# Performance work log

Measured on AMD Instinct MI355X. Metric: run time of the kernel, lower is better.

Reference implementation:

```python
import jax, jax.numpy as jnp
import numpy as np

L, N, C = 128, 32, 128
DIM_MLP, OUT = 128, 128


def setup_inputs() -> dict:
    key = jax.random.key(0)
    ks = jax.random.split(key, 6)
    s_in2 = 1.0 / np.sqrt(2 * C)
    s_mid = 1.0 / np.sqrt(DIM_MLP)
    s_in = 1.0 / np.sqrt(C)
    return {
        "x": jax.random.normal(ks[0], (L, N, C), jnp.float32),
        "attn_w1": jax.random.normal(ks[1], (2 * C, DIM_MLP), jnp.float32) * s_in2,
        "attn_b1": jnp.zeros((DIM_MLP,), jnp.float32),
        "attn_w2": jax.random.normal(ks[2], (DIM_MLP, OUT), jnp.float32) * s_mid,
        "attn_b2": jnp.zeros((OUT,), jnp.float32),
        "value_w1": jax.random.normal(ks[3], (C, DIM_MLP), jnp.float32) * s_in,
        "value_b1": jnp.zeros((DIM_MLP,), jnp.float32),
        "value_w2": jax.random.normal(ks[4], (DIM_MLP, OUT), jnp.float32) * s_mid,
        "value_b2": jnp.zeros((OUT,), jnp.float32),
    }


def reference(x, attn_w1, attn_b1, attn_w2, attn_b2,
              value_w1, value_b1, value_w2, value_b2):
    l, n, c = x.shape
    # Outer concat: pair[i, j, b] = concat(x[i, b], x[j, b])  -> (l, l, N, 2C)
    xi = jnp.broadcast_to(x[:, None, :, :], (l, l, n, c))
    xj = jnp.broadcast_to(x[None, :, :, :], (l, l, n, c))
    pair = jnp.concatenate([xi, xj], axis=-1)
    # Pairwise attention MLP (ReLU hidden, linear output)
    h = jax.nn.relu(pair @ attn_w1 + attn_b1)          # (l, l, N, dim_mlp)
    attn = h @ attn_w2 + attn_b2                       # (l, l, N, out)
    # Value MLP
    hv = jax.nn.relu(x @ value_w1 + value_b1)          # (l, N, dim_mlp)
    value = hv @ value_w2 + value_b2                   # (l, N, out)
    # Elementwise weighted reduce over key axis j (NOT a matmul over channels)
    out = jnp.einsum('ijbc,jbc->ibc', attn, value)     # (l, N, out)
    return out
```

## Files before the change

kernel.cpp:

```cpp
#include <hip/hip_runtime.h>
#include <hip/hip_bf16.h>

#define L_DIM 128
#define N_DIM 32
#define C_DIM 128
#define K_DIM 128
#define OUT_DIM 128

#define QV_STRIDE 132

typedef __attribute__((ext_vector_type(8))) short short8;
typedef __attribute__((ext_vector_type(4))) float float4v;

static __device__ __forceinline__ short bf16_bits(float f) {
    __bf16 h = (__bf16)f;
    return __builtin_bit_cast(short, h);
}

__global__ __launch_bounds__(256) void k_pre(
    const float* __restrict__ x,
    const float* __restrict__ attn_w1, const float* __restrict__ attn_b1,
    const float* __restrict__ attn_w2,
    const float* __restrict__ value_w1, const float* __restrict__ value_b1,
    const float* __restrict__ value_w2, const float* __restrict__ value_b2,
    float* __restrict__ P, float* __restrict__ Q, float* __restrict__ V,
    short* __restrict__ W2s)
{
    int bid = blockIdx.x;
    if (bid >= 256) {
        int e = (bid - 256) * 256 + threadIdx.x;
        int idx  = e & 7;
        int colr = (e >> 3) & 15;
        int quad = (e >> 7) & 3;
        int mi   = (e >> 9) & 3;
        int ct   = e >> 11;
        int k = quad * 8 + 32 * mi + idx;
        int c = ct * 16 + colr;
        W2s[e] = bf16_bits(attn_w2[k * OUT_DIM + c]);
        return;
    }

    __shared__ float xs[16][C_DIM];
    __shared__ float hvs[16][K_DIM];
    int tid = threadIdx.x;
    int r0  = bid * 16;

    {
        int f = tid * 8;
        int row = f >> 7, c = f & 127;
        *(float4v*)(&xs[row][c])     = *(const float4v*)(x + (r0 + row) * C_DIM + c);
        *(float4v*)(&xs[row][c + 4]) = *(const float4v*)(x + (r0 + row) * C_DIM + c + 4);
    }
    __syncthreads();

    int ks   = tid & 127;
    int half = tid >> 7;

    float pacc[8] = {0,0,0,0,0,0,0,0};
    float qacc[8] = {0,0,0,0,0,0,0,0};
    float hacc[8] = {0,0,0,0,0,0,0,0};
    #pragma unroll 4
    for (int c = 0; c < C_DIM; ++c) {
        float wa = attn_w1[c * K_DIM + ks];
        float wb = attn_w1[(C_DIM + c) * K_DIM + ks];
        float wv = value_w1[c * K_DIM + ks];
        #pragma unroll
        for (int r = 0; r < 8; ++r) {
            float xr = xs[half * 8 + r][c];
            pacc[r] = fmaf(xr, wa, pacc[r]);
            qacc[r] = fmaf(xr, wb, qacc[r]);
            hacc[r] = fmaf(xr, wv, hacc[r]);
        }
    }
    float b1 = attn_b1[ks], vb1 = value_b1[ks];
    #pragma unroll
    for (int r = 0; r < 8; ++r) {
        int rr = r0 + half * 8 + r;
        int i = rr >> 5, bb = rr & 31;
        P[(bb * L_DIM + i) * K_DIM + ks] = pacc[r];
        Q[(bb * L_DIM + i) * K_DIM + ks] = qacc[r] + b1;
        hvs[half * 8 + r][ks] = fmaxf(hacc[r] + vb1, 0.f);
    }
    __syncthreads();

    float vacc[8] = {0,0,0,0,0,0,0,0};
    #pragma unroll 4
    for (int k = 0; k < K_DIM; ++k) {
        float w = value_w2[k * OUT_DIM + ks];
        #pragma unroll
        for (int r = 0; r < 8; ++r)
            vacc[r] = fmaf(hvs[half * 8 + r][k], w, vacc[r]);
    }
    float vb2 = value_b2[ks];
    #pragma unroll
    for (int r = 0; r < 8; ++r) {
        int rr = r0 + half * 8 + r;
        int i = rr >> 5, bb = rr & 31;
        V[(bb * L_DIM + i) * OUT_DIM + ks] = vacc[r] + vb2;
    }
}

__global__ __launch_bounds__(256)
__attribute__((amdgpu_waves_per_eu(2, 2)))
void k_main(
    const float* __restrict__ P, const float* __restrict__ Q,
    const float* __restrict__ V,
    const short* __restrict__ W2s, const float* __restrict__ attn_b2,
    float* __restrict__ out)
{
    __shared__ float Q_lds[2][16 * QV_STRIDE];
    __shared__ float V_lds[2][16 * QV_STRIDE];
    __shared__ float P_lds[8 * K_DIM];

    int b     = blockIdx.x >> 4;
    int itile = blockIdx.x & 15;
    int tid   = threadIdx.x;
    int wave  = tid >> 6;
    int lane  = tid & 63;
    int quad  = lane >> 4;
    int col   = lane & 15;

    short8 bfrag[8][4];
    const short8* w2p = (const short8*)W2s;
    #pragma unroll
    for (int ct = 0; ct < 8; ++ct)
        #pragma unroll
        for (int mi = 0; mi < 4; ++mi)
            bfrag[ct][mi] = w2p[((ct * 4 + mi) * 4 + quad) * 16 + col];

    {
        int f = tid * 4;
        int ii = f >> 7, k = f & 127;
        *(float4v*)&P_lds[f] =
            *(const float4v*)(P + (b * L_DIM + itile * 8 + ii) * K_DIM + k);
    }

    int srow = tid >> 4;
    int sc8  = (tid & 15) * 8;
    const float* Qbase = Q + (size_t)(b * L_DIM) * K_DIM;
    const float* Vbase = V + (size_t)(b * L_DIM) * OUT_DIM;

    {
        const float* qp = Qbase + srow * K_DIM + sc8;
        const float* vp = Vbase + srow * OUT_DIM + sc8;
        float4v qa = *(const float4v*)qp, qb = *(const float4v*)(qp + 4);
        float4v va = *(const float4v*)vp, vb = *(const float4v*)(vp + 4);
        *(float4v*)&Q_lds[0][srow * QV_STRIDE + sc8]     = qa;
        *(float4v*)&Q_lds[0][srow * QV_STRIDE + sc8 + 4] = qb;
        *(float4v*)&V_lds[0][srow * QV_STRIDE + sc8]     = va;
        *(float4v*)&V_lds[0][srow * QV_STRIDE + sc8 + 4] = vb;
    }
    __syncthreads();

    float acc[2][8] = {};
    float sv[8]     = {};

    for (int r = 0; r < 8; ++r) {
        int cur = r & 1;

        short8 af[2][4];
        const float* Qc = &Q_lds[cur][col * QV_STRIDE + quad * 8];
        #pragma unroll
        for (int ksl = 0; ksl < 4; ++ksl) {
            float4v q0 = *(const float4v*)(Qc + ksl * 32);
            float4v q1 = *(const float4v*)(Qc + ksl * 32 + 4);
            #pragma unroll
            for (int ii = 0; ii < 2; ++ii) {
                const float* Pc =
                    &P_lds[(wave * 2 + ii) * K_DIM + ksl * 32 + quad * 8];
                float4v pa = *(const float4v*)Pc;
                float4v pb = *(const float4v*)(Pc + 4);
                float4v sa = pa + q0;
                float4v sb = pb + q1;
                short8 a;
                #pragma unroll
                for (int t = 0; t < 4; ++t) {
                    a[t]     = bf16_bits(fmaxf(sa[t], 0.f));
                    a[t + 4] = bf16_bits(fmaxf(sb[t], 0.f));
                }
                af[ii][ksl] = a;
            }
        }

        float4v nqa, nqb, nva, nvb;
        if (r < 7) {
            const float* qp = Qbase + ((r + 1) * 16 + srow) * K_DIM + sc8;
            const float* vp = Vbase + ((r + 1) * 16 + srow) * OUT_DIM + sc8;
            nqa = *(const float4v*)qp; nqb = *(const float4v*)(qp + 4);
            nva = *(const float4v*)vp; nvb = *(const float4v*)(vp + 4);
        }

        const float* Vc = &V_lds[cur][0];
        #pragma unroll
        for (int ct = 0; ct < 8; ++ct) {
            float4v c0 = {0.f, 0.f, 0.f, 0.f};
            float4v c1 = {0.f, 0.f, 0.f, 0.f};
            #pragma unroll
            for (int ksl = 0; ksl < 4; ++ksl) {
                c0 = __builtin_amdgcn_mfma_f32_16x16x32_bf16(
                        af[0][ksl], bfrag[ct][ksl], c0, 0, 0, 0);
                c1 = __builtin_amdgcn_mfma_f32_16x16x32_bf16(
                        af[1][ksl], bfrag[ct][ksl], c1, 0, 0, 0);
            }
            int cc = ct * 16 + col;
            #pragma unroll
            for (int rr = 0; rr < 4; ++rr) {
                float v = Vc[(quad * 4 + rr) * QV_STRIDE + cc];
                acc[0][ct] = fmaf(c0[rr], v, acc[0][ct]);
                acc[1][ct] = fmaf(c1[rr], v, acc[1][ct]);
                sv[ct] += v;
            }
        }

        if (r < 7) {
            int nxt = cur ^ 1;
            *(float4v*)&Q_lds[nxt][srow * QV_STRIDE + sc8]     = nqa;
            *(float4v*)&Q_lds[nxt][srow * QV_STRIDE + sc8 + 4] = nqb;
            *(float4v*)&V_lds[nxt][srow * QV_STRIDE + sc8]     = nva;
            *(float4v*)&V_lds[nxt][srow * QV_STRIDE + sc8 + 4] = nvb;
            __syncthreads();
        }
    }

    #pragma unroll
    for (int ct = 0; ct < 8; ++ct) {
        acc[0][ct] += __shfl_xor(acc[0][ct], 16, 64);
        acc[0][ct] += __shfl_xor(acc[0][ct], 32, 64);
        acc[1][ct] += __shfl_xor(acc[1][ct], 16, 64);
        acc[1][ct] += __shfl_xor(acc[1][ct], 32, 64);
        sv[ct]     += __shfl_xor(sv[ct], 16, 64);
        sv[ct]     += __shfl_xor(sv[ct], 32, 64);
    }

    int ig = itile * 8 + wave * 2 + (quad >> 1);
    #pragma unroll
    for (int ct = 0; ct < 8; ++ct) {
        float a = (quad < 2) ? acc[0][ct] : acc[1][ct];
        if ((quad & 1) == (ct >> 2)) {
            int cc = ct * 16 + col;
            out[(ig * N_DIM + b) * OUT_DIM + cc] =
                a + attn_b2[cc] * sv[ct];
        }
    }
}

extern "C" void kernel_launch(void* const* d_in, const int* in_sizes, int n_in,
                              void* d_out, int out_size, void* d_ws, size_t ws_size,
                              hipStream_t stream)
{
    const float* x        = (const float*)d_in[0];
    const float* attn_w1  = (const float*)d_in[1];
    const float* attn_b1  = (const float*)d_in[2];
    const float* attn_w2  = (const float*)d_in[3];
    const float* attn_b2  = (const float*)d_in[4];
    const float* value_w1 = (const float*)d_in[5];
    const float* value_b1 = (const float*)d_in[6];
    const float* value_w2 = (const float*)d_in[7];
    const float* value_b2 = (const float*)d_in[8];
    float* out = (float*)d_out;

    float* ws  = (float*)d_ws;
    float* P   = ws;
    float* Q   = ws + 524288;
    float* V   = ws + 1048576;
    short* W2s = (short*)(ws + 1572864);

    k_pre<<<320, 256, 0, stream>>>(x, attn_w1, attn_b1, attn_w2,
                                   value_w1, value_b1, value_w2, value_b2,
                                   P, Q, V, W2s);
    k_main<<<512, 256, 0, stream>>>(P, Q, V, W2s, attn_b2, out);
}
```

Measured before the change: 147.6 us.

## Split main kernel across more blocks and waves, stage A fragments in LDS

Main kernel now runs 2048 blocks of 512 threads, with each block handling 2 query rows instead of 8. Each wave handles 2 of the 8 output column tiles instead of all 8. The ReLU(P+Q) A-operand is computed once per element and written to LDS with an XOR swizzle, then read back by the waves as MFMA fragments. This cuts per-wave register pressure (the B fragments drop from 32 to 8 short8) and removes redundant A recomputation, aiming for more occupancy. In exchange it adds an extra barrier per iteration and re-streams Q/V per block. The pre-kernel is also retiled to 8 rows per block for more parallelism.

Result: faster. 132.3 us (-10.3%).

```diff
diff --git a/kernel.cpp b/kernel.cpp
--- a/kernel.cpp
+++ b/kernel.cpp
@@ -27,8 +27,8 @@
     short* __restrict__ W2s)
 {
     int bid = blockIdx.x;
-    if (bid >= 256) {
-        int e = (bid - 256) * 256 + threadIdx.x;
+    if (bid >= 512) {
+        int e = (bid - 512) * 256 + threadIdx.x;
         int idx  = e & 7;
         int colr = (e >> 3) & 15;
         int quad = (e >> 7) & 3;
@@ -40,33 +40,32 @@
         return;
     }
 
-    __shared__ float xs[16][C_DIM];
-    __shared__ float hvs[16][K_DIM];
+    __shared__ float xs[8][C_DIM];
+    __shared__ float hvs[8][K_DIM];
     int tid = threadIdx.x;
-    int r0  = bid * 16;
+    int r0  = bid * 8;
 
     {
-        int f = tid * 8;
+        int f = tid * 4;
         int row = f >> 7, c = f & 127;
-        *(float4v*)(&xs[row][c])     = *(const float4v*)(x + (r0 + row) * C_DIM + c);
-        *(float4v*)(&xs[row][c + 4]) = *(const float4v*)(x + (r0 + row) * C_DIM + c + 4);
+        *(float4v*)(&xs[row][c]) = *(const float4v*)(x + (r0 + row) * C_DIM + c);
     }
     __syncthreads();
 
     int ks   = tid & 127;
     int half = tid >> 7;
 
-    float pacc[8] = {0,0,0,0,0,0,0,0};
-    float qacc[8] = {0,0,0,0,0,0,0,0};
-    float hacc[8] = {0,0,0,0,0,0,0,0};
+    float pacc[4] = {0,0,0,0};
+    float qacc[4] = {0,0,0,0};
+    float hacc[4] = {0,0,0,0};
     #pragma unroll 4
     for (int c = 0; c < C_DIM; ++c) {
         float wa = attn_w1[c * K_DIM + ks];
         float wb = attn_w1[(C_DIM + c) * K_DIM + ks];
         float wv = value_w1[c * K_DIM + ks];
         #pragma unroll
-        for (int r = 0; r < 8; ++r) {
-            float xr = xs[half * 8 + r][c];
+        for (int r = 0; r < 4; ++r) {
+            float xr = xs[half * 4 + r][c];
             pacc[r] = fmaf(xr, wa, pacc[r]);
             qacc[r] = fmaf(xr, wb, qacc[r]);
             hacc[r] = fmaf(xr, wv, hacc[r]);
@@ -74,173 +73,156 @@
     }
     float b1 = attn_b1[ks], vb1 = value_b1[ks];
     #pragma unroll
-    for (int r = 0; r < 8; ++r) {
-        int rr = r0 + half * 8 + r;
+    for (int r = 0; r < 4; ++r) {
+        int rr = r0 + half * 4 + r;
         int i = rr >> 5, bb = rr & 31;
         P[(bb * L_DIM + i) * K_DIM + ks] = pacc[r];
         Q[(bb * L_DIM + i) * K_DIM + ks] = qacc[r] + b1;
-        hvs[half * 8 + r][ks] = fmaxf(hacc[r] + vb1, 0.f);
+        hvs[half * 4 + r][ks] = fmaxf(hacc[r] + vb1, 0.f);
     }
     __syncthreads();
 
-    float vacc[8] = {0,0,0,0,0,0,0,0};
+    float vacc[4] = {0,0,0,0};
     #pragma unroll 4
     for (int k = 0; k < K_DIM; ++k) {
         float w = value_w2[k * OUT_DIM + ks];
         #pragma unroll
-        for (int r = 0; r < 8; ++r)
-            vacc[r] = fmaf(hvs[half * 8 + r][k], w, vacc[r]);
+        for (int r = 0; r < 4; ++r)
+            vacc[r] = fmaf(hvs[half * 4 + r][k], w, vacc[r]);
     }
     float vb2 = value_b2[ks];
     #pragma unroll
-    for (int r = 0; r < 8; ++r) {
-        int rr = r0 + half * 8 + r;
+    for (int r = 0; r < 4; ++r) {
+        int rr = r0 + half * 4 + r;
         int i = rr >> 5, bb = rr & 31;
         V[(bb * L_DIM + i) * OUT_DIM + ks] = vacc[r] + vb2;
     }
 }
 
-__global__ __launch_bounds__(256)
-__attribute__((amdgpu_waves_per_eu(2, 2)))
+__global__ __launch_bounds__(512, 4)
 void k_main(
     const float* __restrict__ P, const float* __restrict__ Q,
     const float* __restrict__ V,
     const short* __restrict__ W2s, const float* __restrict__ attn_b2,
     float* __restrict__ out)
 {
+    __shared__ short A_lds[2 * 256 * 8];
     __shared__ float Q_lds[2][16 * QV_STRIDE];
     __shared__ float V_lds[2][16 * QV_STRIDE];
-    __shared__ float P_lds[8 * K_DIM];
-
-    int b     = blockIdx.x >> 4;
-    int itile = blockIdx.x & 15;
+    __shared__ float P_lds[2 * K_DIM];
+
+    int b     = blockIdx.x >> 6;
+    int ipair = blockIdx.x & 63;
     int tid   = threadIdx.x;
     int wave  = tid >> 6;
     int lane  = tid & 63;
     int quad  = lane >> 4;
     int col   = lane & 15;
-
-    short8 bfrag[8][4];
+    int iw    = wave >> 2;
+    int ctq   = wave & 3;
+
+    short8 bfrag[2][4];
     const short8* w2p = (const short8*)W2s;
     #pragma unroll
-    for (int ct = 0; ct < 8; ++ct)
+    for (int cl = 0; cl < 2; ++cl)
         #pragma unroll
         for (int mi = 0; mi < 4; ++mi)
-            bfrag[ct][mi] = w2p[((ct * 4 + mi) * 4 + quad) * 16 + col];
-
-    {
-        int f = tid * 4;
-        int ii = f >> 7, k = f & 127;
-        *(float4v*)&P_lds[f] =
-            *(const float4v*)(P + (b * L_DIM + itile * 8 + ii) * K_DIM + k);
-    }
-
-    int srow = tid >> 4;
-    int sc8  = (tid & 15) * 8;
+            bfrag[cl][mi] = w2p[(((ctq * 2 + cl) * 4 + mi) * 4 + quad) * 16 + col];
+
+    if (tid < 64)
+        *(float4v*)&P_lds[tid * 4] =
+            *(const float4v*)(P + (b * L_DIM + ipair * 2 + (tid >> 5)) * K_DIM
+                              + (tid & 31) * 4);
+
+    int srow = tid >> 5;
+    int sc   = (tid & 31) * 4;
     const float* Qbase = Q + (size_t)(b * L_DIM) * K_DIM;
     const float* Vbase = V + (size_t)(b * L_DIM) * OUT_DIM;
 
     {
-        const float* qp = Qbase + srow * K_DIM + sc8;
-        const float* vp = Vbase + srow * OUT_DIM + sc8;
-        float4v qa = *(const float4v*)qp, qb = *(const float4v*)(qp + 4);
-        float4v va = *(const float4v*)vp, vb = *(const float4v*)(vp + 4);
-        *(float4v*)&Q_lds[0][srow * QV_STRIDE + sc8]     = qa;
-        *(float4v*)&Q_lds[0][srow * QV_STRIDE + sc8 + 4] = qb;
-        *(float4v*)&V_lds[0][srow * QV_STRIDE + sc8]     = va;
-        *(float4v*)&V_lds[0][srow * QV_STRIDE + sc8 + 4] = vb;
+        float4v q4 = *(const float4v*)(Qbase + srow * K_DIM + sc);
+        float4v v4 = *(const float4v*)(Vbase + srow * OUT_DIM + sc);
+        *(float4v*)&Q_lds[0][srow * QV_STRIDE + sc] = q4;
+        *(float4v*)&V_lds[0][srow * QV_STRIDE + sc] = v4;
     }
     __syncthreads();
 
-    float acc[2][8] = {};
-    float sv[8]     = {};
+    int bi = tid >> 8;
+    int bj = (tid >> 4) & 15;
+    int bk = tid & 15;
+
+    float acc0 = 0.f, acc1 = 0.f, sv0 = 0.f, sv1 = 0.f;
+    int cc0 = ctq * 32 + col;
+    int cc1 = cc0 + 16;
 
     for (int r = 0; r < 8; ++r) {
         int cur = r & 1;
 
-        short8 af[2][4];
-        const float* Qc = &Q_lds[cur][col * QV_STRIDE + quad * 8];
-        #pragma unroll
-        for (int ksl = 0; ksl < 4; ++ksl) {
-            float4v q0 = *(const float4v*)(Qc + ksl * 32);
-            float4v q1 = *(const float4v*)(Qc + ksl * 32 + 4);
+        {
+            const float* Qc = &Q_lds[cur][bj * QV_STRIDE + bk * 8];
+            float4v q0 = *(const float4v*)Qc;
+            float4v q1 = *(const float4v*)(Qc + 4);
+            const float* Pc = &P_lds[bi * K_DIM + bk * 8];
+            float4v p0 = *(const float4v*)Pc;
+            float4v p1 = *(const float4v*)(Pc + 4);
+            float4v s0 = p0 + q0;
+            float4v s1 = p1 + q1;
+            short8 a;
             #pragma unroll
-            for (int ii = 0; ii < 2; ++ii) {
-                const float* Pc =
-                    &P_lds[(wave * 2 + ii) * K_DIM + ksl * 32 + quad * 8];
-                float4v pa = *(const float4v*)Pc;
-                float4v pb = *(const float4v*)(Pc + 4);
-                float4v sa = pa + q0;
-                float4v sb = pb + q1;
-                short8 a;
-                #pragma unroll
-                for (int t = 0; t < 4; ++t) {
-                    a[t]     = bf16_bits(fmaxf(sa[t], 0.f));
-                    a[t + 4] = bf16_bits(fmaxf(sb[t], 0.f));
-                }
-                af[ii][ksl] = a;
+            for (int t = 0; t < 4; ++t) {
+                a[t]     = bf16_bits(fmaxf(s0[t], 0.f));
+                a[t + 4] = bf16_bits(fmaxf(s1[t], 0.f));
             }
-        }
-
-        float4v nqa, nqb, nva, nvb;
+            *(short8*)&A_lds[(bi * 256 + bk * 16 + (bj ^ bk)) * 8] = a;
+        }
+
+        float4v nq, nv;
         if (r < 7) {
-            const float* qp = Qbase + ((r + 1) * 16 + srow) * K_DIM + sc8;
-            const float* vp = Vbase + ((r + 1) * 16 + srow) * OUT_DIM + sc8;
-            nqa = *(const float4v*)qp; nqb = *(const float4v*)(qp + 4);
-            nva = *(const float4v*)vp; nvb = *(const float4v*)(vp + 4);
-        }
-
+            nq = *(const float4v*)(Qbase + ((r + 1) * 16 + srow) * K_DIM + sc);
+            nv = *(const float4v*)(Vbase + ((r + 1) * 16 + srow) * OUT_DIM + sc);
+        }
+
+        __syncthreads();
+
+        int nxt = cur ^ 1;
+        if (r < 7) {
+            *(float4v*)&Q_lds[nxt][srow * QV_STRIDE + sc] = nq;
+            *(float4v*)&V_lds[nxt][srow * QV_STRIDE + sc] = nv;
+        }
+
+        float4v c40 = {0.f, 0.f, 0.f, 0.f};
+        float4v c41 = {0.f, 0.f, 0.f, 0.f};
+        #pragma unroll
+        for (int ks = 0; ks < 4; ++ks) {
+            int kq = ks * 4 + quad;
+            short8 af = *(const short8*)
+                &A_lds[(iw * 256 + kq * 16 + (col ^ kq)) * 8];
+            c40 = __builtin_amdgcn_mfma_f32_16x16x32_bf16(
+                    af, bfrag[0][ks], c40, 0, 0, 0);
+            c41 = __builtin_amdgcn_mfma_f32_16x16x32_bf16(
+                    af, bfrag[1][ks], c41, 0, 0, 0);
+        }
         const float* Vc = &V_lds[cur][0];
         #pragma unroll
-        for (int ct = 0; ct < 8; ++ct) {
-            float4v c0 = {0.f, 0.f, 0.f, 0.f};
-            float4v c1 = {0.f, 0.f, 0.f, 0.f};
-            #pragma unroll
-            for (int ksl = 0; ksl < 4; ++ksl) {
-                c0 = __builtin_amdgcn_mfma_f32_16x16x32_bf16(
-                        af[0][ksl], bfrag[ct][ksl], c0, 0, 0, 0);
-                c1 = __builtin_amdgcn_mfma_f32_16x16x32_bf16(
-                        af[1][ksl], bfrag[ct][ksl], c1, 0, 0, 0);
-            }
-            int cc = ct * 16 + col;
-            #pragma unroll
-            for (int rr = 0; rr < 4; ++rr) {
-                float v = Vc[(quad * 4 + rr) * QV_STRIDE + cc];
-                acc[0][ct] = fmaf(c0[rr], v, acc[0][ct]);
-                acc[1][ct] = fmaf(c1[rr], v, acc[1][ct]);
-                sv[ct] += v;
-            }
-        }
-
-        if (r < 7) {
-            int nxt = cur ^ 1;
-            *(float4v*)&Q_lds[nxt][srow * QV_STRIDE + sc8]     = nqa;
-            *(float4v*)&Q_lds[nxt][srow * QV_STRIDE + sc8 + 4] = nqb;
-            *(float4v*)&V_lds[nxt][srow * QV_STRIDE + sc8]     = nva;
-            *(float4v*)&V_lds[nxt][srow * QV_STRIDE + sc8 + 4] = nvb;
-            __syncthreads();
-        }
-    }
-
-    #pragma unroll
-    for (int ct = 0; ct < 8; ++ct) {
-        acc[0][ct] += __shfl_xor(acc[0][ct], 16, 64);
-        acc[0][ct] += __shfl_xor(acc[0][ct], 32, 64);
-        acc[1][ct] += __shfl_xor(acc[1][ct], 16, 64);
-        acc[1][ct] += __shfl_xor(acc[1][ct], 32, 64);
-        sv[ct]     += __shfl_xor(sv[ct], 16, 64);
-        sv[ct]     += __shfl_xor(sv[ct], 32, 64);
-    }
-
-    int ig = itile * 8 + wave * 2 + (quad >> 1);
-    #pragma unroll
-    for (int ct = 0; ct < 8; ++ct) {
-        float a = (quad < 2) ? acc[0][ct] : acc[1][ct];
-        if ((quad & 1) == (ct >> 2)) {
-            int cc = ct * 16 + col;
-            out[(ig * N_DIM + b) * OUT_DIM + cc] =
-                a + attn_b2[cc] * sv[ct];
-        }
+        for (int rr = 0; rr < 4; ++rr) {
+            float v0 = Vc[(quad * 4 + rr) * QV_STRIDE + cc0];
+            float v1 = Vc[(quad * 4 + rr) * QV_STRIDE + cc1];
+            acc0 = fmaf(c40[rr], v0, acc0);  sv0 += v0;
+            acc1 = fmaf(c41[rr], v1, acc1);  sv1 += v1;
+        }
+
+        __syncthreads();
+    }
+
+    acc0 += __shfl_xor(acc0, 16, 64);  acc0 += __shfl_xor(acc0, 32, 64);
+    acc1 += __shfl_xor(acc1, 16, 64);  acc1 += __shfl_xor(acc1, 32, 64);
+    sv0  += __shfl_xor(sv0, 16, 64);   sv0  += __shfl_xor(sv0, 32, 64);
+    sv1  += __shfl_xor(sv1, 16, 64);   sv1  += __shfl_xor(sv1, 32, 64);
+
+    if (quad == 0) {
+        int ig = ipair * 2 + iw;
+        out[(ig * N_DIM + b) * OUT_DIM + cc0] = acc0 + attn_b2[cc0] * sv0;
+        out[(ig * N_DIM + b) * OUT_DIM + cc1] = acc1 + attn_b2[cc1] * sv1;
     }
 }
 
@@ -265,8 +247,8 @@
     float* V   = ws + 1048576;
     short* W2s = (short*)(ws + 1572864);
 
-    k_pre<<<320, 256, 0, stream>>>(x, attn_w1, attn_b1, attn_w2,
+    k_pre<<<576, 256, 0, stream>>>(x, attn_w1, attn_b1, attn_w2,
                                    value_w1, value_b1, value_w2, value_b2,
                                    P, Q, V, W2s);
-    k_main<<<512, 256, 0, stream>>>(P, Q, V, W2s, attn_b2, out);
-}
+    k_main<<<2048, 512, 0, stream>>>(P, Q, V, W2s, attn_b2, out);
+}
```
